# Kernel tuning notes

Measured on AMD Instinct MI355X. Metric: run time of the kernel, lower is better.

Reference implementation:

```python
import jax, jax.numpy as jnp
import numpy as np

FILTER_ORDER = 49   # M; window length M+1 = 50
FRAME_PERIOD = 80   # samples per frame
TAYLOR_ORDER = 20
B, N_FRAMES = 8, 2000
T = N_FRAMES * FRAME_PERIOD  # 160000


def linear_intpl(c, P):
    """Frame-to-sample linear interpolation (replicate last frame).
    c: (B, N, D) -> (B, N*P, D), matching diffsptk LinearInterpolation
    (align_corners linear upsampling of N+1 replicate-padded points)."""
    cp = jnp.concatenate([c, c[:, -1:, :]], axis=1)              # (B, N+1, D)
    w = (jnp.arange(P, dtype=c.dtype) / P)[None, None, :, None]  # (1,1,P,1)
    out = cp[:, :-1, None, :] * (1 - w) + cp[:, 1:, None, :] * w # (B,N,P,D)
    return out.reshape(c.shape[0], -1, c.shape[-1])


def setup_inputs() -> dict:
    key = jax.random.key(0)
    k1, k2 = jax.random.split(key)
    x = jax.random.normal(k1, (B, T), dtype=jnp.float32)
    # scale cepstra so exp-Taylor stays well-conditioned (realistic magnitudes)
    mc = 0.1 * jax.random.normal(k2, (B, N_FRAMES, FILTER_ORDER + 1), dtype=jnp.float32)
    return {"x": x, "mc": mc}


def reference(x, mc):
    M = FILTER_ORDER
    # alpha=gamma=0 => mgc2c is identity: c = mc
    c0 = mc[..., :1]                               # gain (B, N, 1)
    c = mc.at[..., 0].set(0.0)[..., ::-1]          # remove gain, minimum-phase flip
    c = linear_intpl(c, FRAME_PERIOD)              # (B, T, M+1) per-sample coeffs

    idx = jnp.arange(x.shape[-1])[:, None] + jnp.arange(M + 1)[None, :]  # (T, M+1)

    def step(carry, a):
        xa, y = carry
        xp = jnp.pad(xa, ((0, 0), (M, 0)))         # causal left pad
        xw = xp[:, idx]                            # (B, T, M+1) sliding windows
        xn = jnp.einsum('btk,btk->bt', xw, c) / a  # time-varying FIR + 1/a
        return (xn, y + xn), None

    (_, y), _ = jax.lax.scan(
        step, (x, x), jnp.arange(1, TAYLOR_ORDER + 1, dtype=x.dtype))

    K = jnp.exp(linear_intpl(c0, FRAME_PERIOD))[..., 0]  # (B, T) gain
    return y * K
```

## Files before the change

### kernel.cpp

```cpp
#include <hip/hip_runtime.h>


#define FO    49
#define FP    80
#define NST   20
#define NB    8
#define TT    160000
#define NFR   2000
#define NC    50
#define HALO  1024
#define NT    768
#define NTH   384
#define RPT   8
#define EE    6144
#define TOUT  5120
#define TILES 32
#define PADW  56
#define NFRL  78
#define TROW  100
#define NTC   10

__device__ __forceinline__ int swz(int g) { return g ^ ((g >> 3) & 7); }

__global__ __launch_bounds__(NT, 3) void mlsa_kernel(
    const float* __restrict__ x, const float* __restrict__ mc,
    float* __restrict__ out) {
  __shared__ __align__(16) float sb0[PADW + EE];
  __shared__ __align__(16) float sb1[PADW + EE];
  __shared__ __align__(16) float taps[NFRL * TROW];

  const int tid  = threadIdx.x;
  const int b    = blockIdx.x >> 5;
  const int tile = blockIdx.x & 31;
  const int base = tile * TOUT - HALO;
  const float* __restrict__ xb  = x + b * TT;
  const float* __restrict__ mcb = mc + b * NFR * NC;

  if (tid < PADW) { sb0[tid] = 0.f; sb1[tid] = 0.f; }

  #pragma unroll
  for (int i = 0; i < EE / 4 / NT; ++i) {
    const int q  = i * NT + tid;
    const int t0 = base + q * 4;
    float4 v = make_float4(0.f, 0.f, 0.f, 0.f);
    if (t0 >= 0 && t0 < TT) v = *(const float4*)(xb + t0);
    *(float4*)(sb0 + PADW + 4 * swz(q)) = v;
  }

  const int fb = max(base, 0) / FP;
  for (int idx = tid; idx < NFRL * FO; idx += NT) {
    const int e  = idx / FO;
    const int dm = idx - e * FO;
    const int fa = min(fb + e, NFR - 1);
    const int fn = min(fb + e + 1, NFR - 1);
    const float a0 = mcb[fa * NC + dm + 1];
    const float a1 = mcb[fn * NC + dm + 1];
    *(float2*)(taps + e * TROW + 2 * dm) = make_float2(a0, (a1 - a0) * (1.0f / FP));
  }

  const int P  = (tid >= NTH) ? 1 : 0;
  const int K  = tid - P * NTH;
  const int g0 = base + 16 * K + 8 * P;
  const int gc = min(max(g0, 0), TT - 1);
  const int n0 = gc / FP;
  const int fi = n0 - fb;
  const float p0f = (float)(gc - n0 * FP);

  const int GB = 4 * K - 13 + 2 * P;
  int widx[13];
  #pragma unroll
  for (int i = 0; i < 13; ++i) {
    const int q = GB + i;
    widx[i] = (q < 0) ? (PADW + 4 * q) : (PADW + 4 * swz(q));
  }
  const int sidx0 = PADW + 4 * swz(4 * K + 2 * P);
  const int sidx1 = PADW + 4 * swz(4 * K + 2 * P + 1);

  float xp[RPT];
  #pragma unroll
  for (int k = 0; k < 2; ++k) {
    const int t0 = g0 + 4 * k;
    float4 v = make_float4(0.f, 0.f, 0.f, 0.f);
    if (t0 >= 0 && t0 < TT) v = *(const float4*)(xb + t0);
    xp[4*k] = v.x; xp[4*k+1] = v.y; xp[4*k+2] = v.z; xp[4*k+3] = v.w;
  }
  float y[RPT];
  #pragma unroll
  for (int j = 0; j < RPT; ++j) y[j] = xp[j];

  __syncthreads();

  const float* trow = taps + fi * TROW;
  float4 tr[NTC];
  #pragma unroll
  for (int p = 0; p < NTC; ++p) tr[p] = *(const float4*)(trow + 4 * p);

  const float* rb = sb0;
  float*       wb = sb1;
  #pragma unroll 1
  for (int s = 1; s <= NST; ++s) {
    float A[52];
    #pragma unroll
    for (int i = 0; i < 13; ++i) {
      const float4 v = *(const float4*)(rb + widx[i]);
      A[4*i] = v.x; A[4*i+1] = v.y; A[4*i+2] = v.z; A[4*i+3] = v.w;
    }
    float acc0[RPT], acc1[RPT];
    #pragma unroll
    for (int j = 0; j < RPT; ++j) { acc0[j] = 0.f; acc1[j] = 0.f; }
    #pragma unroll
    for (int p = 0; p < NTC; ++p) {
      const float4 tp = tr[p];
      const int d0 = 2 * p + 1, d1 = 2 * p + 2;
      #pragma unroll
      for (int j = 0; j < RPT; ++j) {
        const int ka = 52 + j - d0;
        const float va = (ka < 52) ? A[ka] : xp[ka - 52];
        acc0[j] = fmaf(tp.x, va, acc0[j]);
        acc1[j] = fmaf(tp.y, va, acc1[j]);
        const int kb = 52 + j - d1;
        const float vb = (kb < 52) ? A[kb] : xp[kb - 52];
        acc0[j] = fmaf(tp.z, vb, acc0[j]);
        acc1[j] = fmaf(tp.w, vb, acc1[j]);
      }
    }
    #pragma unroll
    for (int p = NTC; p < 25; ++p) {
      const float4 tp = *(const float4*)(trow + 4 * p);
      const int d0 = 2 * p + 1, d1 = 2 * p + 2;
      #pragma unroll
      for (int j = 0; j < RPT; ++j) {
        const int ka = 52 + j - d0;
        const float va = (ka < 52) ? A[ka] : xp[ka - 52];
        acc0[j] = fmaf(tp.x, va, acc0[j]);
        acc1[j] = fmaf(tp.y, va, acc1[j]);
        if (d1 <= FO) {
          const int kb = 52 + j - d1;
          const float vb = (kb < 52) ? A[kb] : xp[kb - 52];
          acc0[j] = fmaf(tp.z, vb, acc0[j]);
          acc1[j] = fmaf(tp.w, vb, acc1[j]);
        }
      }
    }
    const float ia = 1.0f / (float)s;
    #pragma unroll
    for (int j = 0; j < RPT; ++j) {
      const float xn = fmaf(p0f + (float)j, acc1[j], acc0[j]) * ia;
      y[j] += xn;
      xp[j] = xn;
    }
    {
      float4 v;
      v.x = xp[0]; v.y = xp[1]; v.z = xp[2]; v.w = xp[3];
      *(float4*)(wb + sidx0) = v;
      v.x = xp[4]; v.y = xp[5]; v.z = xp[6]; v.w = xp[7];
      *(float4*)(wb + sidx1) = v;
    }
    __syncthreads();
    const float* t = rb; rb = wb; wb = (float*)t;
  }

  if (K >= HALO / 16 && g0 < TT) {
    const int n1 = min(n0 + 1, NFR - 1);
    const float k0 = mcb[n0 * NC];
    const float k1 = mcb[n1 * NC];
    const float dk = (k1 - k0) * (1.0f / FP);
    float* ob = out + b * TT + g0;
    #pragma unroll
    for (int k = 0; k < 2; ++k) {
      float4 v;
      #pragma unroll
      for (int e = 0; e < 4; ++e) {
        const int j = 4 * k + e;
        const float Kg = __expf(fmaf(p0f + (float)j, dk, k0));
        ((float*)&v)[e] = y[j] * Kg;
      }
      *(float4*)(ob + 4 * k) = v;
    }
  }
}

extern "C" void kernel_launch(void* const* d_in, const int* in_sizes, int n_in,
                              void* d_out, int out_size, void* d_ws, size_t ws_size,
                              hipStream_t stream) {
  const float* x  = (const float*)d_in[0];
  const float* mc = (const float*)d_in[1];
  float* out      = (float*)d_out;
  mlsa_kernel<<<NB * TILES, NT, 0, stream>>>(x, mc, out);
}
```

Baseline: 81.10 us.

## Use contiguous per-thread sample mapping, stream window loads, cache more taps

Each thread now owns eight contiguous samples (g0 = base + 8*tid) instead of interleaved half-block pairs, which makes neighbouring threads' windows overlap and simplifies indexing. The 13 window float4 loads from LDS are no longer issued in a block up front; they are spread through the tap loop just before each group is first needed, which lowers peak register pressure. That freed register budget is spent on keeping 20 tap float4s in registers instead of 10, cutting LDS tap reads per stage. The risk is higher register use at launch bounds of 3 blocks per CU, which could spill, and LDS bank patterns change with the new mapping.

```diff
diff --git a/kernel.cpp b/kernel.cpp
--- a/kernel.cpp
+++ b/kernel.cpp
@@ -10,7 +10,6 @@
 #define NC    50
 #define HALO  1024
 #define NT    768
-#define NTH   384
 #define RPT   8
 #define EE    6144
 #define TOUT  5120
@@ -18,7 +17,7 @@
 #define PADW  56
 #define NFRL  78
 #define TROW  100
-#define NTC   10
+#define NTC   20
 
 __device__ __forceinline__ int swz(int g) { return g ^ ((g >> 3) & 7); }
 
@@ -58,23 +57,20 @@
     *(float2*)(taps + e * TROW + 2 * dm) = make_float2(a0, (a1 - a0) * (1.0f / FP));
   }
 
-  const int P  = (tid >= NTH) ? 1 : 0;
-  const int K  = tid - P * NTH;
-  const int g0 = base + 16 * K + 8 * P;
+  const int g0 = base + RPT * tid;
   const int gc = min(max(g0, 0), TT - 1);
   const int n0 = gc / FP;
   const int fi = n0 - fb;
   const float p0f = (float)(gc - n0 * FP);
 
-  const int GB = 4 * K - 13 + 2 * P;
   int widx[13];
   #pragma unroll
   for (int i = 0; i < 13; ++i) {
-    const int q = GB + i;
+    const int q = 2 * tid - 13 + i;
     widx[i] = (q < 0) ? (PADW + 4 * q) : (PADW + 4 * swz(q));
   }
-  const int sidx0 = PADW + 4 * swz(4 * K + 2 * P);
-  const int sidx1 = PADW + 4 * swz(4 * K + 2 * P + 1);
+  const int sidx0 = PADW + 4 * swz(2 * tid);
+  const int sidx1 = PADW + 4 * swz(2 * tid + 1);
 
   float xp[RPT];
   #pragma unroll
@@ -100,33 +96,24 @@
   #pragma unroll 1
   for (int s = 1; s <= NST; ++s) {
     float A[52];
-    #pragma unroll
-    for (int i = 0; i < 13; ++i) {
-      const float4 v = *(const float4*)(rb + widx[i]);
-      A[4*i] = v.x; A[4*i+1] = v.y; A[4*i+2] = v.z; A[4*i+3] = v.w;
-    }
     float acc0[RPT], acc1[RPT];
     #pragma unroll
     for (int j = 0; j < RPT; ++j) { acc0[j] = 0.f; acc1[j] = 0.f; }
     #pragma unroll
-    for (int p = 0; p < NTC; ++p) {
-      const float4 tp = tr[p];
-      const int d0 = 2 * p + 1, d1 = 2 * p + 2;
-      #pragma unroll
-      for (int j = 0; j < RPT; ++j) {
-        const int ka = 52 + j - d0;
-        const float va = (ka < 52) ? A[ka] : xp[ka - 52];
-        acc0[j] = fmaf(tp.x, va, acc0[j]);
-        acc1[j] = fmaf(tp.y, va, acc1[j]);
-        const int kb = 52 + j - d1;
-        const float vb = (kb < 52) ? A[kb] : xp[kb - 52];
-        acc0[j] = fmaf(tp.z, vb, acc0[j]);
-        acc1[j] = fmaf(tp.w, vb, acc1[j]);
+    for (int p = 0; p < 25; ++p) {
+      if (p == 0) {
+        const float4 v12 = *(const float4*)(rb + widx[12]);
+        A[48] = v12.x; A[49] = v12.y; A[50] = v12.z; A[51] = v12.w;
+        const float4 v11 = *(const float4*)(rb + widx[11]);
+        A[44] = v11.x; A[45] = v11.y; A[46] = v11.z; A[47] = v11.w;
+      } else if ((p & 1) == 0 && p <= 22) {
+        const int g = 11 - p / 2;
+        const float4 v = *(const float4*)(rb + widx[g]);
+        A[4*g] = v.x; A[4*g+1] = v.y; A[4*g+2] = v.z; A[4*g+3] = v.w;
       }
-    }
-    #pragma unroll
-    for (int p = NTC; p < 25; ++p) {
-      const float4 tp = *(const float4*)(trow + 4 * p);
+      float4 tp;
+      if (p < NTC) tp = tr[p];
+      else         tp = *(const float4*)(trow + 4 * p);
       const int d0 = 2 * p + 1, d1 = 2 * p + 2;
       #pragma unroll
       for (int j = 0; j < RPT; ++j) {
@@ -160,7 +147,7 @@
     const float* t = rb; rb = wb; wb = (float*)t;
   }
 
-  if (K >= HALO / 16 && g0 < TT) {
+  if (tid >= HALO / RPT && g0 < TT) {
     const int n1 = min(n0 + 1, NFR - 1);
     const float k0 = mcb[n0 * NC];
     const float k1 = mcb[n1 * NC];
```

After: 210.4 us. +159.5%, slower.
